# Optimization experiments

Hardware: AMD Instinct MI355X
Metric: run time of the kernel (lower is better)

Reference implementation:

```python
import jax, jax.numpy as jnp
import numpy as np

# Fixed production-scale sizes (equal-sized graphs so unbatch == reshape)
B, NQ, ND = 64, 32, 512     # graph pairs, query nodes/graph, data nodes/graph
DIN, D, K = 64, 128, 16     # GCN_in_size, GCN_out_size, NTN_k
DEG = 8                     # average degree


def _gcn(x, src, dst, W, b):
    """GCNConv with self loops + symmetric normalization (PyG semantics)."""
    N = x.shape[0]
    loop = jnp.arange(N)
    s = jnp.concatenate([src, loop])
    t = jnp.concatenate([dst, loop])
    deg = jax.ops.segment_sum(jnp.ones_like(t, x.dtype), t, num_segments=N)
    dinv = jnp.where(deg > 0, deg ** -0.5, 0.0)
    norm = (dinv[s] * dinv[t])[:, None]
    h = x @ W
    return jax.ops.segment_sum(h[s] * norm, t, num_segments=N) + b


def _three_gcn(x, ei, W1, b1, W2, b2, W3, b3):
    src, dst = ei[0], ei[1]
    h1 = jax.nn.relu(_gcn(x, src, dst, W1, b1))
    h2 = jax.nn.relu(_gcn(h1, src, dst, W2, b2))
    h3 = jax.nn.relu(_gcn(h2, src, dst, W3, b3))
    return h1, h2, h3


def _level(q, d, Wn, Vn, bn, cw, cb):
    """att_layer + NTN + elementwise mult + 1x1 conv + softmax over data nodes.
    q: [B,NQ,D], d: [B,ND,D] -> (softmaxed map [B,NQ,ND], raw map, he [B,K,NQ,ND])."""
    att = jax.nn.softmax(jnp.einsum('bqd,bnd->bqn', q, d) / jnp.sqrt(jnp.float32(D)), axis=-1)
    qW = jnp.einsum('bqd,kde->bkqe', q, Wn)           # [B,K,NQ,D]
    bil = jnp.einsum('bkqe,bne->bkqn', qW, d)          # [B,K,NQ,ND]
    lq = jnp.einsum('kd,bqd->bkq', Vn[:, :D], q)[:, :, :, None]
    ld = jnp.einsum('kd,bnd->bkn', Vn[:, D:], d)[:, :, None, :]
    he = jax.nn.sigmoid(bil + lq + ld + bn[None, :, None, None]) * att[:, None]
    e_raw = jnp.einsum('k,bkqn->bqn', cw, he) + cb     # 1x1 Conv2d(K->1)
    return jax.nn.softmax(e_raw, axis=-1), e_raw, he


def reference(x_d, edge_index_d, x_q, edge_index_q, batch_index_d, batch_index_q,
              W1, b1, W2, b2, W3, b3,
              Wn1, Vn1, bn1, cw1, cb1,
              Wn2, Vn2, bn2, cw2, cb2,
              Wn3, Vn3, bn3, cw3, cb3,
              w_end, b_end):
    d1, d2, d3 = _three_gcn(x_d, edge_index_d, W1, b1, W2, b2, W3, b3)
    q1, q2, q3 = _three_gcn(x_q, edge_index_q, W1, b1, W2, b2, W3, b3)
    # unbatch: batch indices are sorted with equal graph sizes -> reshape
    d1, d2, d3 = (t.reshape(B, ND, D) for t in (d1, d2, d3))
    q1, q2, q3 = (t.reshape(B, NQ, D) for t in (q1, q2, q3))
    e1, _, he1 = _level(q1, d1, Wn1, Vn1, bn1, cw1, cb1)
    _, e2raw, he2 = _level(q2, d2, Wn2, Vn2, bn2, cw2, cb2)
    e3, _, he3 = _level(q3, d3, Wn3, Vn3, bn3, cw3, cb3)
    # Faithful to source quirks: the zip unpack `e1,e2,e3,h1,h2,h1` rebinds h1 to
    # he_3 (he_1 is never used, he_3 appears twice) and end2 enters the concat
    # PRE-softmax (the softmaxed version was assigned to unused `nd2`).
    stack = jnp.concatenate([e1[:, None], e2raw[:, None], e3[:, None], he3, he2, he3], axis=1)
    out = jnp.einsum('c,bcqn->bqn', w_end, stack) + b_end  # con_end 1x1 conv + squeeze
    return jax.nn.softmax(out, axis=-1)                    # softmax over data nodes


def setup_inputs() -> dict:
    key = jax.random.key(0)
    k = jax.random.split(key, 40)
    n = jax.random.normal
    Nd, Nq = B * ND, B * NQ
    Ed, Eq = Nd * DEG, Nq * DEG
    gid_d = jnp.repeat(jnp.arange(B), ND * DEG)
    gid_q = jnp.repeat(jnp.arange(B), NQ * DEG)
    inp = {
        'x_d': n(k[0], (Nd, DIN), jnp.float32),
        'x_q': n(k[1], (Nq, DIN), jnp.float32),
        'edge_index_d': jnp.stack([jax.random.randint(k[2], (Ed,), 0, ND) + gid_d * ND,
                                   jax.random.randint(k[3], (Ed,), 0, ND) + gid_d * ND]),
        'edge_index_q': jnp.stack([jax.random.randint(k[4], (Eq,), 0, NQ) + gid_q * NQ,
                                   jax.random.randint(k[5], (Eq,), 0, NQ) + gid_q * NQ]),
        'batch_index_d': jnp.repeat(jnp.arange(B), ND),
        'batch_index_q': jnp.repeat(jnp.arange(B), NQ),
        'W1': n(k[6], (DIN, D), jnp.float32) / np.sqrt(DIN), 'b1': jnp.zeros((D,), jnp.float32),
        'W2': n(k[7], (D, D), jnp.float32) / np.sqrt(D), 'b2': jnp.zeros((D,), jnp.float32),
        'W3': n(k[8], (D, D), jnp.float32) / np.sqrt(D), 'b3': jnp.zeros((D,), jnp.float32),
    }
    for i, l in enumerate(('1', '2', '3')):
        inp['Wn' + l] = n(k[10 + 4 * i], (K, D, D), jnp.float32) / np.sqrt(D)
        inp['Vn' + l] = n(k[11 + 4 * i], (K, 2 * D), jnp.float32) / np.sqrt(2 * D)
        inp['bn' + l] = jnp.zeros((K,), jnp.float32)
        inp['cw' + l] = n(k[12 + 4 * i], (K,), jnp.float32) / np.sqrt(K)
        inp['cb' + l] = jnp.zeros((1,), jnp.float32)
    inp['w_end'] = n(k[25], (3 * K + 3,), jnp.float32) / np.sqrt(3 * K + 3)
    inp['b_end'] = jnp.zeros((1,), jnp.float32)
    return inp
```

## Files before the change

### kernel.cpp

```cpp
#include <hip/hip_runtime.h>
#include <math.h>

namespace {
constexpr int cB  = 64;
constexpr int cNQ = 32;
constexpr int cND = 512;
constexpr int cNd = cB * cND;
constexpr int cNq = cB * cNQ;
constexpr int cEd = cNd * 8;
constexpr int cEq = cNq * 8;
constexpr int LD_STRIDE = 516;
constexpr int NB_CVT = 2188, NB_T2BF = 808, NB_CNT = (cEd + cEq) / 256;
constexpr int NB_FILL = (cEd + cEq) / 256;
}

#define F4C(p) (*(const float4*)(p))
#define F4W(p) (*(float4*)(p))

typedef __attribute__((ext_vector_type(8))) __bf16 bf16x8;
typedef __attribute__((ext_vector_type(4))) float floatx4;

__device__ __forceinline__ ushort f2bf(float f) {
  union { float f; unsigned u; } v;
  v.f = f;
  unsigned u = v.u;
  return (ushort)((u + 0x7fffu + ((u >> 16) & 1u)) >> 16);
}
__device__ __forceinline__ float bf2f(ushort u) {
  union { unsigned u; float f; } v;
  v.u = ((unsigned)u) << 16;
  return v.f;
}
__device__ __forceinline__ float4 us4f4(ushort4 u) {
  return make_float4(bf2f(u.x), bf2f(u.y), bf2f(u.z), bf2f(u.w));
}
__device__ __forceinline__ ushort4 f4us4(float4 f) {
  ushort4 o;
  o.x = f2bf(f.x); o.y = f2bf(f.y); o.z = f2bf(f.z); o.w = f2bf(f.w);
  return o;
}
__device__ __forceinline__ float fexp2(float x) {
#if __has_builtin(__builtin_amdgcn_exp2f)
  return __builtin_amdgcn_exp2f(x);
#else
  return exp2f(x);
#endif
}
__device__ __forceinline__ float frcp(float x) {
#if __has_builtin(__builtin_amdgcn_rcpf)
  return __builtin_amdgcn_rcpf(x);
#else
  return 1.0f / x;
#endif
}
__device__ __forceinline__ float fsigmoid(float z) {
  return frcp(1.0f + fexp2(z * -1.4426950408889634f));
}
__device__ __forceinline__ float fexp(float x) { return fexp2(x * 1.4426950408889634f); }

__device__ __forceinline__ int swz_g(int j) { return (((j >> 3) & 7) << 3) | (j & 7); }

__global__ __launch_bounds__(256) void k_front(
    const float* __restrict__ xd, const float* __restrict__ xq,
    const float* __restrict__ v0, const float* __restrict__ v1,
    const float* __restrict__ v2, ushort* __restrict__ oxd, ushort* __restrict__ oxq,
    ushort* __restrict__ ov0, ushort* __restrict__ ov1, ushort* __restrict__ ov2,
    const float* __restrict__ W1, const float* __restrict__ W2,
    const float* __restrict__ W3, const float* __restrict__ Wn0,
    const float* __restrict__ Wn1, const float* __restrict__ Wn2,
    ushort* __restrict__ o1, ushort* __restrict__ o2, ushort* __restrict__ o3,
    ushort* __restrict__ on0, ushort* __restrict__ on1, ushort* __restrict__ on2,
    const int* __restrict__ dst_d, const int* __restrict__ dst_q,
    int* __restrict__ cnt_d, int* __restrict__ cnt_q) {
  __shared__ float tile[32][33];
  int blk = blockIdx.x, tid = threadIdx.x;
  if (blk < NB_CVT) {
    const float* src;
    ushort* dst;
    int i;
    if (blk < 2048) { src = xd; dst = oxd; i = blk * 256 + tid; }
    else if (blk < 2176) { src = xq; dst = oxq; i = (blk - 2048) * 256 + tid; }
    else if (blk < 2180) { src = v0; dst = ov0; i = (blk - 2176) * 256 + tid; }
    else if (blk < 2184) { src = v1; dst = ov1; i = (blk - 2180) * 256 + tid; }
    else { src = v2; dst = ov2; i = (blk - 2184) * 256 + tid; }
    *(ushort4*)(dst + (size_t)i * 4) = f4us4(F4C(src + (size_t)i * 4));
  } else if (blk < NB_CVT + NB_T2BF) {
    int b5 = blk - NB_CVT;
    const float* in;
    ushort* out;
    int R, C, bt, t;
    if (b5 < 8)        { in = W1;  out = o1;  R = 64;  C = 128; bt = 0; t = b5; }
    else if (b5 < 24)  { in = W2;  out = o2;  R = 128; C = 128; bt = 0; t = b5 - 8; }
    else if (b5 < 40)  { in = W3;  out = o3;  R = 128; C = 128; bt = 0; t = b5 - 24; }
    else if (b5 < 296) { in = Wn0; out = on0; R = 128; C = 128; bt = (b5 - 40) >> 4;  t = (b5 - 40) & 15; }
    else if (b5 < 552) { in = Wn1; out = on1; R = 128; C = 128; bt = (b5 - 296) >> 4; t = (b5 - 296) & 15; }
    else               { in = Wn2; out = on2; R = 128; C = 128; bt = (b5 - 552) >> 4; t = (b5 - 552) & 15; }
    int tilesC = C >> 5;
    int tr = t / tilesC, tc = t - tr * tilesC;
    int tx = tid & 31, ty = tid >> 5;
    const float* ib = in + (size_t)bt * R * C;
    ushort* ob = out + (size_t)bt * R * C;
#pragma unroll
    for (int i = 0; i < 4; ++i)
      tile[ty + i * 8][tx] = ib[(tr * 32 + ty + i * 8) * C + tc * 32 + tx];
    __syncthreads();
#pragma unroll
    for (int i = 0; i < 4; ++i)
      ob[(size_t)(tc * 32 + ty + i * 8) * R + tr * 32 + tx] = f2bf(tile[tx][ty + i * 8]);
  } else {
    int i = (blk - NB_CVT - NB_T2BF) * 256 + tid;
    if (i < cEd) atomicAdd(&cnt_d[dst_d[i]], 1);
    else atomicAdd(&cnt_q[dst_q[i - cEd]], 1);
  }
}

__global__ __launch_bounds__(512) void k_scan_dinv(
    const int* __restrict__ cnt_d, const int* __restrict__ cnt_q,
    int* __restrict__ rp_d, int* __restrict__ rp_q,
    float* __restrict__ dinv_d, float* __restrict__ dinv_q) {
  __shared__ int sh[512];
  int blk = blockIdx.x, tid = threadIdx.x;
  if (blk < 64) {
    int v = cnt_d[blk * 512 + tid];
    sh[tid] = v;
    __syncthreads();
    for (int off = 1; off < 512; off <<= 1) {
      int t = (tid >= off) ? sh[tid - off] : 0;
      __syncthreads();
      sh[tid] += t;
      __syncthreads();
    }
    rp_d[blk * 512 + tid] = blk * 4096 + sh[tid] - v;
  } else if (blk < 68) {
    int g = (blk - 64) * 16 + (tid >> 5);
    int lane32 = tid & 31;
    int v = cnt_q[g * 32 + lane32];
    int incl = v;
#pragma unroll
    for (int off = 1; off < 32; off <<= 1) {
      int t = __shfl_up(incl, off, 32);
      if (lane32 >= off) incl += t;
    }
    rp_q[g * 32 + lane32] = g * 256 + incl - v;
  } else {
    int i = (blk - 68) * 512 + tid;
    if (i < cNd) dinv_d[i] = 1.0f / sqrtf((float)(cnt_d[i] + 1));
    else dinv_q[i - cNd] = 1.0f / sqrtf((float)(cnt_q[i - cNd] + 1));
  }
}

__global__ __launch_bounds__(256) void k_fill_gemm1(
    const int* __restrict__ src_d, const int* __restrict__ dst_d,
    const int* __restrict__ src_q, const int* __restrict__ dst_q,
    const int* __restrict__ rp_d, const int* __restrict__ rp_q,
    int* __restrict__ cur_d, int* __restrict__ cur_q, int* __restrict__ col_d,
    int* __restrict__ col_q, const ushort* __restrict__ xdbf,
    const ushort* __restrict__ xqbf, const ushort* __restrict__ w1T,
    const float* __restrict__ dinv_d, const float* __restrict__ dinv_q,
    ushort* __restrict__ htmp) {
  int blk = blockIdx.x, tid = threadIdx.x;
  if (blk < NB_FILL) {
    int i = blk * 256 + tid;
    if (i < cEd) {
      int d = dst_d[i];
      int p = atomicAdd(&cur_d[d], 1);
      col_d[rp_d[d] + p] = src_d[i];
    } else {
      int j = i - cEd;
      int d = dst_q[j];
      int p = atomicAdd(&cur_q[d], 1);
      col_q[rp_q[d] + p] = src_q[j];
    }
    return;
  }
  int blk2 = blk - NB_FILL;
  int wave = tid >> 6, lane = tid & 63;
  int col = lane & 15, quad = lane >> 4;
  bool isQ = blk2 >= 512;
  int node0;
  if (isQ) node0 = (blk2 - 512) * 64;
  else node0 = swz_g(blk2) * 512 + (blk2 >> 6) * 64;
  int mloc = node0 + wave * 16;
  const ushort* X = isQ ? xqbf : xdbf;
  const float* dv = isQ ? dinv_q : dinv_d;
  size_t hbase = isQ ? (size_t)cNd : 0;
  floatx4 acc[8];
#pragma unroll
  for (int ct = 0; ct < 8; ++ct)
#pragma unroll
    for (int r = 0; r < 4; ++r) acc[ct][r] = 0.0f;
#pragma unroll
  for (int kc = 0; kc < 2; ++kc) {
    bf16x8 a = *(const bf16x8*)(X + (size_t)(mloc + col) * 64 + kc * 32 + quad * 8);
#pragma unroll
    for (int ct = 0; ct < 8; ++ct) {
      bf16x8 b = *(const bf16x8*)(w1T + (size_t)(ct * 16 + col) * 64 + kc * 32 + quad * 8);
      acc[ct] = __builtin_amdgcn_mfma_f32_16x16x32_bf16(a, b, acc[ct], 0, 0, 0);
    }
  }
  float sc[4];
#pragma unroll
  for (int r = 0; r < 4; ++r) sc[r] = dv[mloc + quad * 4 + r];
#pragma unroll
  for (int ct = 0; ct < 8; ++ct)
#pragma unroll
    for (int r = 0; r < 4; ++r)
      htmp[(hbase + mloc + quad * 4 + r) * 128 + ct * 16 + col] = f2bf(acc[ct][r] * sc[r]);
}

__global__ __launch_bounds__(256) void gmn_gather_merged(
    const ushort* __restrict__ htmp, const int* __restrict__ rp_d,
    const int* __restrict__ cnt_d, const int* __restrict__ col_d,
    const float* __restrict__ dinv_d, const int* __restrict__ rp_q,
// ... 342 lines not shown
#pragma unroll
      for (int r = 0; r < 4; ++r) s_red[(quad * 4 + r) * 8 + wave] = red[r];
    __syncthreads();
#pragma unroll
    for (int r = 0; r < 4; ++r) {
      float m = s_red[(quad * 4 + r) * 8];
#pragma unroll
      for (int w = 1; w < 8; ++w) m += s_red[(quad * 4 + r) * 8 + w];
      M[r] = frcp(m);
    }
    __syncthreads();
#pragma unroll
    for (int s = 0; s < 4; ++s)
#pragma unroll
      for (int r = 0; r < 4; ++r) eacc[s][r] *= M[r];
  }
  float w = w_end[widx];
#pragma unroll
  for (int s = 0; s < 4; ++s)
#pragma unroll
    for (int r = 0; r < 4; ++r) eacc[s][r] = w * eacc[s][r] + (hasF ? facc[s][r] : 0.0f);

  if (mode == 0) {
#pragma unroll
    for (int s = 0; s < 4; ++s)
#pragma unroll
      for (int r = 0; r < 4; ++r)
        accb[((size_t)(b * 32 + qh * 16 + quad * 4 + r) << 9) + n0 + s * 16 + col] =
            eacc[s][r];
  } else if (mode == 1) {
#pragma unroll
    for (int s = 0; s < 4; ++s)
#pragma unroll
      for (int r = 0; r < 4; ++r)
        accb[((size_t)(b * 32 + qh * 16 + quad * 4 + r) << 9) + n0 + s * 16 + col] +=
            eacc[s][r];
  } else {
    float be = b_end[0];
#pragma unroll
    for (int s = 0; s < 4; ++s)
#pragma unroll
      for (int r = 0; r < 4; ++r)
        eacc[s][r] += accb[((size_t)(b * 32 + qh * 16 + quad * 4 + r) << 9) +
                           n0 + s * 16 + col] + be;
#pragma unroll
    for (int r = 0; r < 4; ++r) {
      float m = fmaxf(fmaxf(eacc[0][r], eacc[1][r]), fmaxf(eacc[2][r], eacc[3][r]));
#pragma unroll
      for (int o = 1; o < 16; o <<= 1) m = fmaxf(m, __shfl_xor(m, o, 64));
      red[r] = m;
    }
    if (col == 0)
#pragma unroll
      for (int r = 0; r < 4; ++r) s_red[(quad * 4 + r) * 8 + wave] = red[r];
    __syncthreads();
#pragma unroll
    for (int r = 0; r < 4; ++r) {
      float m = s_red[(quad * 4 + r) * 8];
#pragma unroll
      for (int w2 = 1; w2 < 8; ++w2) m = fmaxf(m, s_red[(quad * 4 + r) * 8 + w2]);
      M[r] = m;
    }
    __syncthreads();
#pragma unroll
    for (int s = 0; s < 4; ++s)
#pragma unroll
      for (int r = 0; r < 4; ++r) eacc[s][r] = fexp(eacc[s][r] - M[r]);
#pragma unroll
    for (int r = 0; r < 4; ++r) {
      float m = eacc[0][r] + eacc[1][r] + eacc[2][r] + eacc[3][r];
#pragma unroll
      for (int o = 1; o < 16; o <<= 1) m += __shfl_xor(m, o, 64);
      red[r] = m;
    }
    if (col == 0)
#pragma unroll
      for (int r = 0; r < 4; ++r) s_red[(quad * 4 + r) * 8 + wave] = red[r];
    __syncthreads();
#pragma unroll
    for (int r = 0; r < 4; ++r) {
      float m = s_red[(quad * 4 + r) * 8];
#pragma unroll
      for (int w2 = 1; w2 < 8; ++w2) m += s_red[(quad * 4 + r) * 8 + w2];
      M[r] = frcp(m);
    }
#pragma unroll
    for (int s = 0; s < 4; ++s)
#pragma unroll
      for (int r = 0; r < 4; ++r)
        out[((size_t)(b * 32 + qh * 16 + quad * 4 + r) << 9) + n0 + s * 16 + col] =
            eacc[s][r] * M[r];
  }
}

extern "C" void kernel_launch(void* const* d_in, const int* in_sizes, int n_in,
                              void* d_out, int out_size, void* d_ws, size_t ws_size,
                              hipStream_t stream) {
  (void)in_sizes; (void)n_in; (void)out_size; (void)ws_size;
  const float* x_d = (const float*)d_in[0];
  const float* x_q = (const float*)d_in[1];
  const int* ei_d = (const int*)d_in[2];
  const int* ei_q = (const int*)d_in[3];
  const float* W1 = (const float*)d_in[6];
  const float* b1 = (const float*)d_in[7];
  const float* W2 = (const float*)d_in[8];
  const float* b2 = (const float*)d_in[9];
  const float* W3 = (const float*)d_in[10];
  const float* b3 = (const float*)d_in[11];
  const float* Wn[3] = {(const float*)d_in[12], (const float*)d_in[17], (const float*)d_in[22]};
  const float* Vn[3] = {(const float*)d_in[13], (const float*)d_in[18], (const float*)d_in[23]};
  const float* bn[3] = {(const float*)d_in[14], (const float*)d_in[19], (const float*)d_in[24]};
  const float* cw[3] = {(const float*)d_in[15], (const float*)d_in[20], (const float*)d_in[25]};
  const float* w_end = (const float*)d_in[27];
  const float* b_end = (const float*)d_in[28];
  float* out = (float*)d_out;

  char* wsp = (char*)d_ws;
  auto alloc = [&](size_t nbytes) {
    void* p = (void*)wsp;
    wsp += (nbytes + 255) & ~(size_t)255;
    return p;
  };
  int* cnt_d = (int*)alloc(cNd * 4);
  int* cnt_q = (int*)alloc(cNq * 4);
  int* cur_d = (int*)alloc(cNd * 4);
  int* cur_q = (int*)alloc(cNq * 4);
  float* dinv_d = (float*)alloc(cNd * 4);
  float* dinv_q = (float*)alloc(cNq * 4);
  int* rp_d = (int*)alloc(cNd * 4);
  int* rp_q = (int*)alloc(cNq * 4);
  int* col_d = (int*)alloc((size_t)cEd * 4);
  int* col_q = (int*)alloc((size_t)cEq * 4);
  ushort* xdbf = (ushort*)alloc((size_t)cNd * 64 * 2);
  ushort* xqbf = (ushort*)alloc((size_t)cNq * 64 * 2);
  ushort* w1T = (ushort*)alloc(128 * 64 * 2);
  ushort* w2T = (ushort*)alloc(128 * 128 * 2);
  ushort* w3T = (ushort*)alloc(128 * 128 * 2);
  ushort* wnT[3];
  for (int l = 0; l < 3; ++l) wnT[l] = (ushort*)alloc((size_t)16 * 128 * 128 * 2);
  ushort* vnbf[3];
  for (int l = 0; l < 3; ++l) vnbf[l] = (ushort*)alloc(16 * 256 * 2);
  ushort* htmp = (ushort*)alloc((size_t)(cNd + cNq) * 128 * 2);
  ushort* dbf = (ushort*)alloc((size_t)cNd * 128 * 2);
  ushort* qbf[3];
  for (int l = 0; l < 3; ++l) qbf[l] = (ushort*)alloc((size_t)cNq * 128 * 2);
  float* accb = (float*)alloc((size_t)cB * cNQ * cND * 4);
  ushort* qwbuf = (ushort*)alloc((size_t)cB * 16 * 32 * 128 * 2);

  const int* src_d = ei_d;
  const int* dst_d = ei_d + cEd;
  const int* src_q = ei_q;
  const int* dst_q = ei_q + cEq;

  hipMemsetAsync(cnt_d, 0, (size_t)2 * (cNd + cNq) * 4, stream);

  k_front<<<NB_CVT + NB_T2BF + NB_CNT, 256, 0, stream>>>(
      x_d, x_q, Vn[0], Vn[1], Vn[2], xdbf, xqbf, vnbf[0], vnbf[1], vnbf[2], W1, W2,
      W3, Wn[0], Wn[1], Wn[2], w1T, w2T, w3T, wnT[0], wnT[1], wnT[2], dst_d, dst_q,
      cnt_d, cnt_q);

  k_scan_dinv<<<136, 512, 0, stream>>>(cnt_d, cnt_q, rp_d, rp_q, dinv_d, dinv_q);

  k_fill_gemm1<<<NB_FILL + 544, 256, 0, stream>>>(
      src_d, dst_d, src_q, dst_q, rp_d, rp_q, cur_d, cur_q, col_d, col_q, xdbf, xqbf,
      w1T, dinv_d, dinv_q, htmp);

  const float* bias[3] = {b1, b2, b3};
  const ushort* nextWT[3] = {w2T, w3T, nullptr};
  const int o1s[3] = {0, 19, 3};
  const int o2s[3] = {-1, -1, 35};
  const int hasF[3] = {0, 1, 1};
  const int dosms[3] = {1, 0, 1};
  const int modes[3] = {0, 1, 2};

  for (int l = 0; l < 3; ++l) {
    gmn_gather_merged<<<(cNd + cNq) / 8, 256, 0, stream>>>(
        htmp, rp_d, cnt_d, col_d, dinv_d, rp_q, cnt_q, col_q, dinv_q, bias[l], dbf,
        qbf[l]);
    gmn_qw<<<1024, 256, 0, stream>>>(qbf[l], wnT[l], qwbuf);
    int grid = (l < 2) ? (128 + 272) : 128;
    k_level_gemm<<<grid, 512, 0, stream>>>(
        qbf[l], dbf, qwbuf, vnbf[l], bn[l], cw[l], w_end, b_end, o1s[l], o2s[l],
        hasF[l], dosms[l], modes[l], l, accb, out, nextWT[l], dinv_d, dinv_q, htmp);
  }
}
```

Baseline: 300.2 us.

## Fuse all stages into one cooperative persistent kernel with grid syncs

Measured after the change: 686.5 us. +128.7%, slower.

```diff
diff --git a/kernel.cpp b/kernel.cpp
--- a/kernel.cpp
+++ b/kernel.cpp
@@ -1,5 +1,8 @@
 #include <hip/hip_runtime.h>
+#include <hip/hip_cooperative_groups.h>
 #include <math.h>
+
+namespace cg = cooperative_groups;
 
 namespace {
 constexpr int cB  = 64;
@@ -10,12 +13,23 @@
 constexpr int cEd = cNd * 8;
 constexpr int cEq = cNq * 8;
 constexpr int LD_STRIDE = 516;
+
+constexpr int NB = 256;
+constexpr int NT = 512;
+
+constexpr int W_XD = 8192;
+constexpr int W_XQ = 512;
+constexpr int W_V  = 16;
+constexpr int W_CVT = W_XD + W_XQ + 3 * W_V;
+constexpr int W_TR  = 808;
+constexpr int W_TOT = W_CVT + W_TR;
+constexpr int WSLOTS = (NB - 68) * 8;
+
 constexpr int NB_CVT = 2188, NB_T2BF = 808, NB_CNT = (cEd + cEq) / 256;
 constexpr int NB_FILL = (cEd + cEq) / 256;
 }
 
 #define F4C(p) (*(const float4*)(p))
-#define F4W(p) (*(float4*)(p))
 
 typedef __attribute__((ext_vector_type(8))) __bf16 bf16x8;
 typedef __attribute__((ext_vector_type(4))) float floatx4;
@@ -59,6 +73,626 @@
 __device__ __forceinline__ float fexp(float x) { return fexp2(x * 1.4426950408889634f); }
 
 __device__ __forceinline__ int swz_g(int j) { return (((j >> 3) & 7) << 3) | (j & 7); }
+
+struct MP {
+  const float *x_d, *x_q;
+  const int *src_d, *dst_d, *src_q, *dst_q;
+  const float *W1, *W2, *W3, *Wn0, *Wn1, *Wn2, *V0, *V1, *V2;
+  const float *b1, *b2, *b3, *bn0, *bn1, *bn2, *cw0, *cw1, *cw2, *w_end, *b_end;
+  ushort *xdbf, *xqbf, *w1T, *w2T, *w3T, *wnT0, *wnT1, *wnT2;
+  ushort *vnbf0, *vnbf1, *vnbf2;
+  int *cnt_d, *cnt_q, *rp_d, *rp_q;
+  float *dinv_d, *dinv_q;
+  int *col_d, *col_q;
+  ushort *htmp, *dbf, *qbf0, *qbf1, *qbf2, *qwbuf;
+  float *accb, *out;
+};
+
+__global__ __launch_bounds__(512, 2) void k_mega(MP P) {
+  cg::grid_group grid = cg::this_grid();
+  __shared__ __align__(16) char SM[34816];
+  const int tid = threadIdx.x;
+  const int rb = blockIdx.x;
+  const int wave = tid >> 6, lane = tid & 63;
+  const int col = lane & 15, quad = lane >> 4;
+  const int t256 = tid & 255;
+  const int sub = rb * 2 + (tid >> 8);
+
+  if (rb < 64) {
+    int g = rb;
+    const int* dstg = P.dst_d + g * 4096;
+    const int* srcg = P.src_d + g * 4096;
+    int nbase = g * 512;
+    int* s_cnt = (int*)SM;
+    int* s_base = (int*)(SM + 2048);
+    int* s_cur = (int*)(SM + 4096);
+    s_cnt[tid] = 0;
+    __syncthreads();
+    for (int e = tid; e < 4096; e += 512) atomicAdd(&s_cnt[dstg[e] - nbase], 1);
+    __syncthreads();
+    int v = s_cnt[tid];
+    s_base[tid] = v;
+    __syncthreads();
+    for (int off = 1; off < 512; off <<= 1) {
+      int a = (tid >= off) ? s_base[tid - off] : 0;
+      __syncthreads();
+      s_base[tid] += a;
+      __syncthreads();
+    }
+    int excl = s_base[tid] - v;
+    P.cnt_d[nbase + tid] = v;
+    P.rp_d[nbase + tid] = g * 4096 + excl;
+    P.dinv_d[nbase + tid] = 1.0f / sqrtf((float)(v + 1));
+    s_base[tid] = excl;
+    s_cur[tid] = 0;
+    __syncthreads();
+    for (int e = tid; e < 4096; e += 512) {
+      int d = dstg[e] - nbase;
+      int p = atomicAdd(&s_cur[d], 1);
+      P.col_d[g * 4096 + s_base[d] + p] = srcg[e];
+    }
+  } else if (rb < 68) {
+    int lg = tid >> 5, l32 = tid & 31;
+    int g = (rb - 64) * 16 + lg;
+    const int* dstg = P.dst_q + g * 256;
+    const int* srcg = P.src_q + g * 256;
+    int nbase = g * 32;
+    int* s_cnt = (int*)SM;
+    int* s_base = (int*)(SM + 2048);
+    int* s_cur = (int*)(SM + 4096);
+    s_cnt[tid] = 0;
+    __syncthreads();
+#pragma unroll
+    for (int j = 0; j < 8; ++j)
+      atomicAdd(&s_cnt[lg * 32 + (dstg[l32 + j * 32] - nbase)], 1);
+    __syncthreads();
+    int v = s_cnt[tid];
+    int incl = v;
+#pragma unroll
+    for (int off = 1; off < 32; off <<= 1) {
+      int a = __shfl_up(incl, off, 32);
+      if (l32 >= off) incl += a;
+    }
+    int excl = incl - v;
+    P.cnt_q[nbase + l32] = v;
+    P.rp_q[nbase + l32] = g * 256 + excl;
+    P.dinv_q[nbase + l32] = 1.0f / sqrtf((float)(v + 1));
+    s_base[tid] = excl;
+    s_cur[tid] = 0;
+    __syncthreads();
+#pragma unroll
+    for (int j = 0; j < 8; ++j) {
+      int e = l32 + j * 32;
+      int d = dstg[e] - nbase;
+      int p = atomicAdd(&s_cur[lg * 32 + d], 1);
+      P.col_q[g * 256 + s_base[lg * 32 + d] + p] = srcg[e];
+    }
+  } else {
+    int wslot = (rb - 68) * 8 + wave;
+    for (int t = wslot; t < W_TOT; t += WSLOTS) {
+      if (t < W_CVT) {
+        const float* srcp;
+        ushort* dstp;
+        int u;
+        if (t < W_XD) { srcp = P.x_d; dstp = P.xdbf; u = t * 64 + lane; }
+        else if (t < W_XD + W_XQ) { srcp = P.x_q; dstp = P.xqbf; u = (t - W_XD) * 64 + lane; }
+        else if (t < W_XD + W_XQ + W_V) { srcp = P.V0; dstp = P.vnbf0; u = (t - W_XD - W_XQ) * 64 + lane; }
+        else if (t < W_XD + W_XQ + 2 * W_V) { srcp = P.V1; dstp = P.vnbf1; u = (t - W_XD - W_XQ - W_V) * 64 + lane; }
+        else { srcp = P.V2; dstp = P.vnbf2; u = (t - W_XD - W_XQ - 2 * W_V) * 64 + lane; }
+        *(ushort4*)(dstp + (size_t)u * 4) = f4us4(F4C(srcp + (size_t)u * 4));
+      } else {
+        int tt = t - W_CVT;
+        const float* in;
+        ushort* ow;
+        int R, C, bt, tx;
+        if (tt < 8)        { in = P.W1;  ow = P.w1T;  R = 64;  C = 128; bt = 0; tx = tt; }
+        else if (tt < 24)  { in = P.W2;  ow = P.w2T;  R = 128; C = 128; bt = 0; tx = tt - 8; }
+        else if (tt < 40)  { in = P.W3;  ow = P.w3T;  R = 128; C = 128; bt = 0; tx = tt - 24; }
+        else if (tt < 296) { in = P.Wn0; ow = P.wnT0; R = 128; C = 128; bt = (tt - 40) >> 4;  tx = (tt - 40) & 15; }
+        else if (tt < 552) { in = P.Wn1; ow = P.wnT1; R = 128; C = 128; bt = (tt - 296) >> 4; tx = (tt - 296) & 15; }
+        else               { in = P.Wn2; ow = P.wnT2; R = 128; C = 128; bt = (tt - 552) >> 4; tx = (tt - 552) & 15; }
+        int tilesC = C >> 5;
+        int tr = tx / tilesC, tc = tx - tr * tilesC;
+        const float* ib = in + (size_t)bt * R * C;
+        ushort* ob = ow + (size_t)bt * R * C;
+        float* tw = (float*)(SM + wave * 4224);
+        int lx = lane & 31, lh = lane >> 5;
+#pragma unroll
+        for (int i = 0; i < 16; ++i) {
+          int r = lh + 2 * i;
+          tw[r * 33 + lx] = ib[(size_t)(tr * 32 + r) * C + tc * 32 + lx];
+        }
+        asm volatile("s_waitcnt lgkmcnt(0)" ::: "memory");
+#pragma unroll
+        for (int i = 0; i < 16; ++i) {
+          int c = lh + 2 * i;
+          ob[(size_t)(tc * 32 + c) * R + tr * 32 + lx] = f2bf(tw[lx * 33 + c]);
+        }
+        asm volatile("s_waitcnt lgkmcnt(0)" ::: "memory");
+      }
+    }
+  }
+  grid.sync();
+
+  {
+    int w4 = t256 >> 6;
+    for (int s = sub; s < 544; s += 512) {
+      bool isQ = s >= 512;
+      int node0;
+      if (isQ) node0 = (s - 512) * 64;
+      else node0 = swz_g(s) * 512 + (s >> 6) * 64;
+      int mloc = node0 + w4 * 16;
+      const ushort* X = isQ ? P.xqbf : P.xdbf;
+      const float* dv = isQ ? P.dinv_q : P.dinv_d;
+      size_t hbase = isQ ? (size_t)cNd : 0;
+      floatx4 acc[8];
+#pragma unroll
+      for (int ct = 0; ct < 8; ++ct)
+#pragma unroll
+        for (int r = 0; r < 4; ++r) acc[ct][r] = 0.0f;
+#pragma unroll
+      for (int kc = 0; kc < 2; ++kc) {
+        bf16x8 a = *(const bf16x8*)(X + (size_t)(mloc + col) * 64 + kc * 32 + quad * 8);
+#pragma unroll
+        for (int ct = 0; ct < 8; ++ct) {
+          bf16x8 b = *(const bf16x8*)(P.w1T + (size_t)(ct * 16 + col) * 64 + kc * 32 + quad * 8);
+          acc[ct] = __builtin_amdgcn_mfma_f32_16x16x32_bf16(a, b, acc[ct], 0, 0, 0);
+        }
+      }
+      float sc[4];
+#pragma unroll
+      for (int r = 0; r < 4; ++r) sc[r] = dv[mloc + quad * 4 + r];
+#pragma unroll
+      for (int ct = 0; ct < 8; ++ct)
+#pragma unroll
+        for (int r = 0; r < 4; ++r)
+          P.htmp[(hbase + mloc + quad * 4 + r) * 128 + ct * 16 + col] = f2bf(acc[ct][r] * sc[r]);
+    }
+  }
+  grid.sync();
+
+  for (int l = 0; l < 3; ++l) {
+    const ushort* vnbf = l == 0 ? P.vnbf0 : (l == 1 ? P.vnbf1 : P.vnbf2);
+    const float* bnl = l == 0 ? P.bn0 : (l == 1 ? P.bn1 : P.bn2);
+    const float* cwl = l == 0 ? P.cw0 : (l == 1 ? P.cw1 : P.cw2);
+    const ushort* wnTl = l == 0 ? P.wnT0 : (l == 1 ? P.wnT1 : P.wnT2);
+    const float* biasl = l == 0 ? P.b1 : (l == 1 ? P.b2 : P.b3);
+    ushort* qbfl = l == 0 ? P.qbf0 : (l == 1 ? P.qbf1 : P.qbf2);
+    const ushort* gWT = l == 0 ? P.w2T : P.w3T;
+    const int o1 = l == 0 ? 0 : (l == 1 ? 19 : 3);
+    const int o2 = l == 2 ? 35 : -1;
+    const int hasF = l > 0 ? 1 : 0;
+    const int do_sm = (l == 1) ? 0 : 1;
+    const int mode = l;
+    const int widx = l;
+
+    {
+      int l32 = tid & 31;
+      for (int s = sub; s < 4352; s += 512) {
+        bool isQ = s < 256;
+        int node;
+        const int *rp, *cnt, *colv;
+        const float* dinv;
+        const ushort* hs;
+        ushort* outp;
+        if (isQ) {
+          node = swz_g(s & 63) * 32 + (s >> 6) * 8 + (t256 >> 5);
+          rp = P.rp_q; cnt = P.cnt_q; colv = P.col_q; dinv = P.dinv_q;
+          hs = P.htmp + (size_t)cNd * 128;
+          outp = qbfl;
+        } else {
+          int j = s - 256;
+          node = swz_g(j & 63) * 512 + (j >> 6) * 8 + (t256 >> 5);
+          rp = P.rp_d; cnt = P.cnt_d; colv = P.col_d; dinv = P.dinv_d;
+          hs = P.htmp;
+          outp = P.dbf;
+        }
+        int c = cnt[node], s0 = rp[node];
+        float dt = dinv[node];
+        float4 acc = us4f4(*(const ushort4*)(hs + (size_t)node * 128 + l32 * 4));
+        int cm = c < 32 ? c : 32;
+        for (int j0 = 0; j0 < cm; j0 += 8) {
+          int ss[8];
+          ushort4 vv[8];
+#pragma unroll
+          for (int u = 0; u < 8; ++u) {
+            int jj = j0 + u;
+            ss[u] = (jj < cm) ? colv[s0 + jj] : -1;
+          }
+#pragma unroll
+          for (int u = 0; u < 8; ++u)
+            if (ss[u] >= 0) vv[u] = *(const ushort4*)(hs + (size_t)ss[u] * 128 + l32 * 4);
+#pragma unroll
+          for (int u = 0; u < 8; ++u) {
+            if (ss[u] >= 0) {
+              float4 f = us4f4(vv[u]);
+              acc.x += f.x; acc.y += f.y; acc.z += f.z; acc.w += f.w;
+            }
+          }
+        }
+        for (int j2 = 32; j2 < c; ++j2) {
+          int s2 = colv[s0 + j2];
+          float4 f = us4f4(*(const ushort4*)(hs + (size_t)s2 * 128 + l32 * 4));
+          acc.x += f.x; acc.y += f.y; acc.z += f.z; acc.w += f.w;
+        }
+        float4 bv = F4C(biasl + l32 * 4);
+        float4 r;
+        r.x = fmaxf(acc.x * dt + bv.x, 0.0f);
+        r.y = fmaxf(acc.y * dt + bv.y, 0.0f);
+        r.z = fmaxf(acc.z * dt + bv.z, 0.0f);
+        r.w = fmaxf(acc.w * dt + bv.w, 0.0f);
+        *(ushort4*)(outp + (size_t)node * 128 + l32 * 4) = f4us4(r);
+      }
+    }
+    grid.sync();
+
+    {
+      int w4 = t256 >> 6;
+      int et0 = w4 * 2;
+      for (int s = sub; s < 1024; s += 512) {
+        int b = swz_g(s & 63), k = s >> 6;
+        floatx4 acc[2][2];
+#pragma unroll
+        for (int qt = 0; qt < 2; ++qt)
+#pragma unroll
+          for (int ei = 0; ei < 2; ++ei)
+#pragma unroll
+            for (int r = 0; r < 4; ++r) acc[qt][ei][r] = 0.0f;
+#pragma unroll
+        for (int kc = 0; kc < 4; ++kc) {
+          bf16x8 a0 = *(const bf16x8*)(qbfl + (size_t)(b * 32 + col) * 128 + kc * 32 + quad * 8);
+          bf16x8 a1 = *(const bf16x8*)(qbfl + (size_t)(b * 32 + 16 + col) * 128 + kc * 32 + quad * 8);
+#pragma unroll
+          for (int ei = 0; ei < 2; ++ei) {
+            bf16x8 bf = *(const bf16x8*)(wnTl + (size_t)(k * 128 + (et0 + ei) * 16 + col) * 128 +
+                                         kc * 32 + quad * 8);
+            acc[0][ei] = __builtin_amdgcn_mfma_f32_16x16x32_bf16(a0, bf, acc[0][ei], 0, 0, 0);
+            acc[1][ei] = __builtin_amdgcn_mfma_f32_16x16x32_bf16(a1, bf, acc[1][ei], 0, 0, 0);
+          }
+        }
+#pragma unroll
+        for (int qt = 0; qt < 2; ++qt)
+#pragma unroll
+          for (int ei = 0; ei < 2; ++ei)
+#pragma unroll
+            for (int r = 0; r < 4; ++r)
+              P.qwbuf[((size_t)(b * 16 + k) << 12) + (qt * 16 + quad * 4 + r) * 128 +
+                      (et0 + ei) * 16 + col] = f2bf(acc[qt][ei][r]);
+      }
+    }
+    grid.sync();
+
+    if (rb < 128) {
+      float* s_ld = (float*)SM;
+      float* s_lq = (float*)(SM + 33024);
+      float* s_red = (float*)(SM + 34048);
+      int b = swz_g(rb & 63);
+      int qh = rb >> 6;
+      int n0 = wave * 64;
+
+      bf16x8 bfr[4][4];
+#pragma unroll
+      for (int s = 0; s < 4; ++s)
+#pragma unroll
+        for (int kc = 0; kc < 4; ++kc)
+          bfr[s][kc] = *(const bf16x8*)(P.dbf + ((size_t)(b * 512 + n0 + s * 16 + col) << 7) +
+                                        kc * 32 + quad * 8);
+      bf16x8 aq[4];
+#pragma unroll
+      for (int kc = 0; kc < 4; ++kc)
+        aq[kc] = *(const bf16x8*)(qbfl + (size_t)(b * 32 + qh * 16 + col) * 128 +
+                                  kc * 32 + quad * 8);
+
+      floatx4 att[4];
+#pragma unroll
+      for (int s = 0; s < 4; ++s)
+#pragma unroll
+        for (int r = 0; r < 4; ++r) att[s][r] = 0.0f;
+#pragma unroll
+      for (int kc = 0; kc < 4; ++kc)
+#pragma unroll
+        for (int s = 0; s < 4; ++s)
+          att[s] = __builtin_amdgcn_mfma_f32_16x16x32_bf16(aq[kc], bfr[s][kc], att[s], 0, 0, 0);
+      const float sc = 0.088388347648318440550f;
+#pragma unroll
+      for (int s = 0; s < 4; ++s)
+#pragma unroll
+        for (int r = 0; r < 4; ++r) att[s][r] *= sc;
+
+      {
+        bf16x8 vn2[4];
+#pragma unroll
+        for (int kc = 0; kc < 4; ++kc)
+          vn2[kc] = *(const bf16x8*)(vnbf + col * 256 + 128 + kc * 32 + quad * 8);
+#pragma unroll
+        for (int s = 0; s < 4; ++s) {
+          floatx4 lda;
+#pragma unroll
+          for (int r = 0; r < 4; ++r) lda[r] = 0.0f;
+#pragma unroll
+          for (int kc = 0; kc < 4; ++kc)
+            lda = __builtin_amdgcn_mfma_f32_16x16x32_bf16(bfr[s][kc], vn2[kc], lda, 0, 0, 0);
+#pragma unroll
+          for (int r = 0; r < 4; ++r)
+            s_ld[col * LD_STRIDE + n0 + s * 16 + quad * 4 + r] = lda[r];
+        }
+      }
+      if (wave == 0) {
+        bf16x8 vn1[4];
+#pragma unroll
+        for (int kc = 0; kc < 4; ++kc)
+          vn1[kc] = *(const bf16x8*)(vnbf + col * 256 + kc * 32 + quad * 8);
+        floatx4 lqa;
+#pragma unroll
+        for (int r = 0; r < 4; ++r) lqa[r] = 0.0f;
+#pragma unroll
+        for (int kc = 0; kc < 4; ++kc)
+          lqa = __builtin_amdgcn_mfma_f32_16x16x32_bf16(aq[kc], vn1[kc], lqa, 0, 0, 0);
+#pragma unroll
+        for (int r = 0; r < 4; ++r) s_lq[col * 16 + quad * 4 + r] = lqa[r];
+      }
+      __syncthreads();
+
+      float red[4], M[4];
+#pragma unroll
+      for (int r = 0; r < 4; ++r) {
+        float m = fmaxf(fmaxf(att[0][r], att[1][r]), fmaxf(att[2][r], att[3][r]));
+#pragma unroll
+        for (int o = 1; o < 16; o <<= 1) m = fmaxf(m, __shfl_xor(m, o, 64));
+        red[r] = m;
+      }
+      if (col == 0)
+#pragma unroll
+        for (int r = 0; r < 4; ++r) s_red[(quad * 4 + r) * 8 + wave] = red[r];
+      __syncthreads();
+#pragma unroll
+      for (int r = 0; r < 4; ++r) {
+        float m = s_red[(quad * 4 + r) * 8];
+#pragma unroll
+        for (int w = 1; w < 8; ++w) m = fmaxf(m, s_red[(quad * 4 + r) * 8 + w]);
+        M[r] = m;
+      }
+      __syncthreads();
+#pragma unroll
+      for (int s = 0; s < 4; ++s)
+#pragma unroll
+        for (int r = 0; r < 4; ++r) att[s][r] = fexp(att[s][r] - M[r]);
+#pragma unroll
+      for (int r = 0; r < 4; ++r) {
+        float m = att[0][r] + att[1][r] + att[2][r] + att[3][r];
+#pragma unroll
+        for (int o = 1; o < 16; o <<= 1) m += __shfl_xor(m, o, 64);
+        red[r] = m;
+      }
+      if (col == 0)
+#pragma unroll
+        for (int r = 0; r < 4; ++r) s_red[(quad * 4 + r) * 8 + wave] = red[r];
+      __syncthreads();
+#pragma unroll
+      for (int r = 0; r < 4; ++r) {
+        float m = s_red[(quad * 4 + r) * 8];
+#pragma unroll
+        for (int w = 1; w < 8; ++w) m += s_red[(quad * 4 + r) * 8 + w];
+        M[r] = frcp(m);
+      }
+      __syncthreads();
+#pragma unroll
+      for (int s = 0; s < 4; ++s)
+#pragma unroll
+        for (int r = 0; r < 4; ++r) att[s][r] *= M[r];
+
+      floatx4 eacc[4], facc[4];
+#pragma unroll
+      for (int s = 0; s < 4; ++s)
+#pragma unroll
+        for (int r = 0; r < 4; ++r) { eacc[s][r] = 0.0f; facc[s][r] = 0.0f; }
+
+#pragma unroll 4
+      for (int k = 0; k < 16; ++k) {
+        const ushort* qk = P.qwbuf + ((size_t)(b * 16 + k) << 12) + (qh * 16 + col) * 128 + quad * 8;
+        bf16x8 a0 = *(const bf16x8*)(qk);
+        bf16x8 a1 = *(const bf16x8*)(qk + 32);
+        bf16x8 a2 = *(const bf16x8*)(qk + 64);
+        bf16x8 a3 = *(const bf16x8*)(qk + 96);
+        floatx4 bil[4];
+#pragma unroll
+        for (int s = 0; s < 4; ++s) {
+#pragma unroll
+          for (int r = 0; r < 4; ++r) bil[s][r] = 0.0f;
+          bil[s] = __builtin_amdgcn_mfma_f32_16x16x32_bf16(a0, bfr[s][0], bil[s], 0, 0, 0);
+          bil[s] = __builtin_amdgcn_mfma_f32_16x16x32_bf16(a1, bfr[s][1], bil[s], 0, 0, 0);
+          bil[s] = __builtin_amdgcn_mfma_f32_16x16x32_bf16(a2, bfr[s][2], bil[s], 0, 0, 0);
+          bil[s] = __builtin_amdgcn_mfma_f32_16x16x32_bf16(a3, bfr[s][3], bil[s], 0, 0, 0);
+        }
+        float bnk = bnl[k], cwk = cwl[k];
+        float wkk = 0.0f;
+        if (hasF) {
+          wkk = P.w_end[o1 + k];
+          if (o2 >= 0) wkk += P.w_end[o2 + k];
+        }
+        float lqv[4];
+#pragma unroll
+        for (int r = 0; r < 4; ++r) lqv[r] = s_lq[k * 16 + quad * 4 + r] + bnk;
+#pragma unroll
+        for (int s = 0; s < 4; ++s) {
+          float ldv = s_ld[k * LD_STRIDE + n0 + s * 16 + col];
+#pragma unroll
+          for (int r = 0; r < 4; ++r) {
+            float sg = fsigmoid(bil[s][r] + lqv[r] + ldv);
+            eacc[s][r] += cwk * sg;
+            facc[s][r] += wkk * sg;
+          }
+        }
+      }
+
+#pragma unroll
+      for (int s = 0; s < 4; ++s)
+#pragma unroll
+        for (int r = 0; r < 4; ++r) {
+          eacc[s][r] *= att[s][r];
+          facc[s][r] *= att[s][r];
+        }
+      if (do_sm) {
+#pragma unroll
+        for (int r = 0; r < 4; ++r) {
+          float m = fmaxf(fmaxf(eacc[0][r], eacc[1][r]), fmaxf(eacc[2][r], eacc[3][r]));
+#pragma unroll
+          for (int o = 1; o < 16; o <<= 1) m = fmaxf(m, __shfl_xor(m, o, 64));
+          red[r] = m;
+        }
+        if (col == 0)
+#pragma unroll
+          for (int r = 0; r < 4; ++r) s_red[(quad * 4 + r) * 8 + wave] = red[r];
+        __syncthreads();
+#pragma unroll
+        for (int r = 0; r < 4; ++r) {
+          float m = s_red[(quad * 4 + r) * 8];
+#pragma unroll
+          for (int w = 1; w < 8; ++w) m = fmaxf(m, s_red[(quad * 4 + r) * 8 + w]);
+          M[r] = m;
+        }
+        __syncthreads();
+#pragma unroll
+        for (int s = 0; s < 4; ++s)
+#pragma unroll
+          for (int r = 0; r < 4; ++r) eacc[s][r] = fexp(eacc[s][r] - M[r]);
+#pragma unroll
+        for (int r = 0; r < 4; ++r) {
+          float m = eacc[0][r] + eacc[1][r] + eacc[2][r] + eacc[3][r];
+#pragma unroll
+          for (int o = 1; o < 16; o <<= 1) m += __shfl_xor(m, o, 64);
+          red[r] = m;
+        }
+        if (col == 0)
+#pragma unroll
+          for (int r = 0; r < 4; ++r) s_red[(quad * 4 + r) * 8 + wave] = red[r];
+        __syncthreads();
+#pragma unroll
+        for (int r = 0; r < 4; ++r) {
+          float m = s_red[(quad * 4 + r) * 8];
+#pragma unroll
+          for (int w = 1; w < 8; ++w) m += s_red[(quad * 4 + r) * 8 + w];
+          M[r] = frcp(m);
+        }
+        __syncthreads();
+#pragma unroll
+        for (int s = 0; s < 4; ++s)
+#pragma unroll
+          for (int r = 0; r < 4; ++r) eacc[s][r] *= M[r];
+      }
+      float wE = P.w_end[widx];
+#pragma unroll
+      for (int s = 0; s < 4; ++s)
+#pragma unroll
+        for (int r = 0; r < 4; ++r) eacc[s][r] = wE * eacc[s][r] + (hasF ? facc[s][r] : 0.0f);
+
+      if (mode == 0) {
+#pragma unroll
+        for (int s = 0; s < 4; ++s)
+#pragma unroll
+          for (int r = 0; r < 4; ++r)
+            P.accb[((size_t)(b * 32 + qh * 16 + quad * 4 + r) << 9) + n0 + s * 16 + col] =
+                eacc[s][r];
+      } else if (mode == 1) {
+#pragma unroll
+        for (int s = 0; s < 4; ++s)
+#pragma unroll
+          for (int r = 0; r < 4; ++r)
+            P.accb[((size_t)(b * 32 + qh * 16 + quad * 4 + r) << 9) + n0 + s * 16 + col] +=
+                eacc[s][r];
+      } else {
+        float be = P.b_end[0];
+#pragma unroll
+        for (int s = 0; s < 4; ++s)
+#pragma unroll
+          for (int r = 0; r < 4; ++r)
+            eacc[s][r] += P.accb[((size_t)(b * 32 + qh * 16 + quad * 4 + r) << 9) +
+                                 n0 + s * 16 + col] + be;
+#pragma unroll
+        for (int r = 0; r < 4; ++r) {
+          float m = fmaxf(fmaxf(eacc[0][r], eacc[1][r]), fmaxf(eacc[2][r], eacc[3][r]));
+#pragma unroll
+          for (int o = 1; o < 16; o <<= 1) m = fmaxf(m, __shfl_xor(m, o, 64));
+          red[r] = m;
+        }
+        if (col == 0)
+#pragma unroll
+          for (int r = 0; r < 4; ++r) s_red[(quad * 4 + r) * 8 + wave] = red[r];
+        __syncthreads();
+#pragma unroll
+        for (int r = 0; r < 4; ++r) {
+          float m = s_red[(quad * 4 + r) * 8];
+#pragma unroll
+          for (int w2 = 1; w2 < 8; ++w2) m = fmaxf(m, s_red[(quad * 4 + r) * 8 + w2]);
+          M[r] = m;
+        }
+        __syncthreads();
+#pragma unroll
+        for (int s = 0; s < 4; ++s)
+#pragma unroll
+          for (int r = 0; r < 4; ++r) eacc[s][r] = fexp(eacc[s][r] - M[r]);
+#pragma unroll
+        for (int r = 0; r < 4; ++r) {
+          float m = eacc[0][r] + eacc[1][r] + eacc[2][r] + eacc[3][r];
+#pragma unroll
+          for (int o = 1; o < 16; o <<= 1) m += __shfl_xor(m, o, 64);
+          red[r] = m;
+        }
+        if (col == 0)
+#pragma unroll
+          for (int r = 0; r < 4; ++r) s_red[(quad * 4 + r) * 8 + wave] = red[r];
+        __syncthreads();
+#pragma unroll
+        for (int r = 0; r < 4; ++r) {
+          float m = s_red[(quad * 4 + r) * 8];
+#pragma unroll
+          for (int w2 = 1; w2 < 8; ++w2) m += s_red[(quad * 4 + r) * 8 + w2];
+          M[r] = frcp(m);
+        }
+#pragma unroll
+        for (int s = 0; s < 4; ++s)
+#pragma unroll
+          for (int r = 0; r < 4; ++r)
+            P.out[((size_t)(b * 32 + qh * 16 + quad * 4 + r) << 9) + n0 + s * 16 + col] =
+                eacc[s][r] * M[r];
+      }
+    } else if (l < 2) {
+      for (int t = rb - 128; t < 272; t += 128) {
+        bool isQ = t >= 256;
+        int node0;
+        if (isQ) node0 = (t - 256) * 128;
+        else node0 = swz_g(t & 63) * 512 + (t >> 6) * 128;
+        int mloc = node0 + wave * 16;
+        const ushort* X = isQ ? qbfl : P.dbf;
+        const float* dv = isQ ? P.dinv_q : P.dinv_d;
+        size_t hbase = isQ ? (size_t)cNd : 0;
+        floatx4 acc[8];
+#pragma unroll
+        for (int ct = 0; ct < 8; ++ct)
+#pragma unroll
+          for (int r = 0; r < 4; ++r) acc[ct][r] = 0.0f;
+#pragma unroll
+        for (int kc = 0; kc < 4; ++kc) {
+          bf16x8 a = *(const bf16x8*)(X + (size_t)(mloc + col) * 128 + kc * 32 + quad * 8);
+#pragma unroll
+          for (int ct = 0; ct < 8; ++ct) {
+            bf16x8 b = *(const bf16x8*)(gWT + (size_t)(ct * 16 + col) * 128 + kc * 32 + quad * 8);
+            acc[ct] = __builtin_amdgcn_mfma_f32_16x16x32_bf16(a, b, acc[ct], 0, 0, 0);
+          }
+        }
+        float sc2[4];
+#pragma unroll
+        for (int r = 0; r < 4; ++r) sc2[r] = dv[mloc + quad * 4 + r];
+#pragma unroll
+        for (int ct = 0; ct < 8; ++ct)
+#pragma unroll
+          for (int r = 0; r < 4; ++r)
+            P.htmp[(hbase + mloc + quad * 4 + r) * 128 + ct * 16 + col] = f2bf(acc[ct][r] * sc2[r]);
+      }
+    }
+    if (l < 2) grid.sync();
+  }
+}
 
 __global__ __launch_bounds__(256) void k_front(
     const float* __restrict__ xd, const float* __restrict__ xq,
@@ -707,15 +1341,39 @@
   const int* src_q = ei_q;
   const int* dst_q = ei_q + cEq;
 
+  MP P;
+  P.x_d = x_d; P.x_q = x_q;
+  P.src_d = src_d; P.dst_d = dst_d; P.src_q = src_q; P.dst_q = dst_q;
+  P.W1 = W1; P.W2 = W2; P.W3 = W3;
+  P.Wn0 = Wn[0]; P.Wn1 = Wn[1]; P.Wn2 = Wn[2];
+  P.V0 = Vn[0]; P.V1 = Vn[1]; P.V2 = Vn[2];
+  P.b1 = b1; P.b2 = b2; P.b3 = b3;
+  P.bn0 = bn[0]; P.bn1 = bn[1]; P.bn2 = bn[2];
+  P.cw0 = cw[0]; P.cw1 = cw[1]; P.cw2 = cw[2];
+  P.w_end = w_end; P.b_end = b_end;
+  P.xdbf = xdbf; P.xqbf = xqbf;
+  P.w1T = w1T; P.w2T = w2T; P.w3T = w3T;
+  P.wnT0 = wnT[0]; P.wnT1 = wnT[1]; P.wnT2 = wnT[2];
+  P.vnbf0 = vnbf[0]; P.vnbf1 = vnbf[1]; P.vnbf2 = vnbf[2];
+  P.cnt_d = cnt_d; P.cnt_q = cnt_q; P.rp_d = rp_d; P.rp_q = rp_q;
+  P.dinv_d = dinv_d; P.dinv_q = dinv_q;
+  P.col_d = col_d; P.col_q = col_q;
+  P.htmp = htmp; P.dbf = dbf;
+  P.qbf0 = qbf[0]; P.qbf1 = qbf[1]; P.qbf2 = qbf[2];
+  P.qwbuf = qwbuf; P.accb = accb; P.out = out;
+
+  void* kargs[] = {(void*)&P};
+  hipError_t err = hipLaunchCooperativeKernel((const void*)k_mega, dim3(NB), dim3(NT),
+                                              kargs, 0, stream);
+  if (err == hipSuccess) return;
+  (void)hipGetLastError();
+
   hipMemsetAsync(cnt_d, 0, (size_t)2 * (cNd + cNq) * 4, stream);
-
   k_front<<<NB_CVT + NB_T2BF + NB_CNT, 256, 0, stream>>>(
       x_d, x_q, Vn[0], Vn[1], Vn[2], xdbf, xqbf, vnbf[0], vnbf[1], vnbf[2], W1, W2,
       W3, Wn[0], Wn[1], Wn[2], w1T, w2T, w3T, wnT[0], wnT[1], wnT[2], dst_d, dst_q,
       cnt_d, cnt_q);
-
   k_scan_dinv<<<136, 512, 0, stream>>>(cnt_d, cnt_q, rp_d, rp_q, dinv_d, dinv_q);
-
   k_fill_gemm1<<<NB_FILL + 544, 256, 0, stream>>>(
       src_d, dst_d, src_q, dst_q, rp_d, rp_q, cur_d, cur_q, col_d, col_q, xdbf, xqbf,
       w1T, dinv_d, dinv_q, htmp);
@@ -727,7 +1385,6 @@
   const int hasF[3] = {0, 1, 1};
   const int dosms[3] = {1, 0, 1};
   const int modes[3] = {0, 1, 2};
-
   for (int l = 0; l < 3; ++l) {
     gmn_gather_merged<<<(cNd + cNq) / 8, 256, 0, stream>>>(
         htmp, rp_d, cnt_d, col_d, dinv_d, rp_q, cnt_q, col_q, dinv_q, bias[l], dbf,
```
